# Kernel tuning notes

Measured on AMD Instinct MI355X. Metric: run time of the kernel, lower is better.

Reference implementation:

```python
import jax, jax.numpy as jnp
import numpy as np

B, T, D = 8, 512, 1024
S, H, TOPK = 2048, 4, 8
Dh = D // H
LR_FAST, LR_DEEP = 1.0, 0.1
SURPRISE_TH, DECAY = 0.6, 0.9995


def layer_norm(x, g, b, eps=1e-5):
    m = jnp.mean(x, -1, keepdims=True)
    v = jnp.var(x, -1, keepdims=True)
    return (x - m) * jax.lax.rsqrt(v + eps) * g + b


def setup_inputs() -> dict:
    key = jax.random.key(0)
    ks = jax.random.split(key, 8)
    s = 0.02
    f32 = jnp.float32
    return {
        "x": jax.random.normal(ks[0], (B, T, D), f32),
        "write_mask": jnp.ones((B, T), dtype=bool),
        # Mamba backbone stub: 2 residual MLP blocks (Linear d->2d, GELU, Linear 2d->d, LN)
        "W1": jax.random.normal(ks[1], (2, D, 2 * D), f32) * s,
        "b1": jnp.zeros((2, 2 * D), f32),
        "W2": jax.random.normal(ks[2], (2, 2 * D, D), f32) * s,
        "b2": jnp.zeros((2, D), f32),
        "ln_g": jnp.ones((2, D), f32),
        "ln_b": jnp.zeros((2, D), f32),
        # memory fusion
        "fuse_W": jax.random.normal(ks[3], (2 * D, D), f32) * s,
        "fuse_b": jnp.zeros((D,), f32),
        "mln_g": jnp.ones((D,), f32),
        "mln_b": jnp.zeros((D,), f32),
        # persistent DualTierMiras memory bank (keys / values)
        "mem_K": jax.random.normal(ks[4], (S, D), f32) * s,
        "mem_V": jax.random.normal(ks[5], (S, D), f32) * s,
    }


def _forward(x, write_mask, W1, b1, W2, b2, ln_g, ln_b, fuse_W, fuse_b, mln_g, mln_b, mem_K, mem_V):
    # --- Mamba backbone (vectorized over B,T) ---
    h = x
    for i in range(2):
        y = jax.nn.gelu(h @ W1[i] + b1[i]) @ W2[i] + b2[i]
        h = h + layer_norm(y, ln_g[i], ln_b[i])

    inv_sqrt_dh = 1.0 / np.sqrt(Dh).astype(np.float32)
    inv_sqrt_d = 1.0 / np.sqrt(D).astype(np.float32)

    def step(carry, inputs):
        mK, mV = carry                      # [S,D] each
        h_t, m_t = inputs                   # [B,D], [B] bool
        # --- top-k sparse multi-head memory read ---
        q = h_t.reshape(B, H, Dh)
        Kh = mK.reshape(S, H, Dh).transpose(1, 0, 2)   # [H,S,Dh]
        Vh = mV.reshape(S, H, Dh).transpose(1, 0, 2)   # [H,S,Dh]
        scores = jnp.einsum('bhd,hsd->bhs', q, Kh) * inv_sqrt_dh  # [B,H,S]
        topv, topi = jax.lax.top_k(scores, TOPK)                   # [B,H,K]
        w = jax.nn.softmax(topv, axis=-1)
        vals = jax.vmap(lambda v, i: v[i])(Vh, topi.transpose(1, 0, 2))  # [H,B,K,Dh]
        v_t = jnp.einsum('bhk,hbkd->bhd', w, vals).reshape(B, D)
        # --- residual fusion ---
        fused = jnp.concatenate([h_t, v_t], -1) @ fuse_W + fuse_b
        fused = layer_norm(fused + h_t, mln_g, mln_b)
        # --- surprise-gated EMA scatter write (detached, decayed) ---
        key_w = jax.lax.stop_gradient(h_t)
        val_w = jax.lax.stop_gradient(fused)
        sw = key_w @ mK.T * inv_sqrt_d                 # [B,S]
        p = jax.nn.softmax(sw, -1)
        slot = jnp.argmax(sw, -1)                      # [B]
        surprise = 1.0 - jnp.max(p, -1)                # [B]
        lr = jnp.where(surprise > SURPRISE_TH, LR_FAST, LR_DEEP)
        lr = lr * m_t.astype(lr.dtype)                 # per-sample write gate
        decay = jnp.where(jnp.any(m_t), DECAY, 1.0)
        mV2 = mV * decay
        mV2 = mV2.at[slot].add(lr[:, None] * (val_w - mV2[slot]))
        mK2 = mK.at[slot].add(lr[:, None] * (key_w - mK[slot]))
        return (mK2, mV2), fused

    (_, _), out = jax.lax.scan(step, (mem_K, mem_V), (h.transpose(1, 0, 2), write_mask.T))
    return out.transpose(1, 0, 2)   # [B,T,D]


def reference(x, write_mask, W1, b1, W2, b2, ln_g, ln_b, fuse_W, fuse_b, mln_g, mln_b, mem_K, mem_V):
    return _forward(x, write_mask, W1, b1, W2, b2, ln_g, ln_b, fuse_W, fuse_b, mln_g, mln_b, mem_K, mem_V)
```

## Files before the change

### kernel.cpp

```cpp
#include <hip/hip_runtime.h>
#include <cstdint>

#define TT 512
#define DD 1024
#define SS 2048
#define BB 8
#define DECAYF 0.9995f
#define NBLK 80

__device__ __forceinline__ float cldf(const float* p) {
  return __hip_atomic_load(p, __ATOMIC_RELAXED, __HIP_MEMORY_SCOPE_AGENT);
}
__device__ __forceinline__ void cstf(float* p, float v) {
  __hip_atomic_store(p, v, __ATOMIC_RELAXED, __HIP_MEMORY_SCOPE_AGENT);
}
__device__ __forceinline__ int cldi(const int* p) {
  return __hip_atomic_load(p, __ATOMIC_RELAXED, __HIP_MEMORY_SCOPE_AGENT);
}
__device__ __forceinline__ void csti(int* p, int v) {
  __hip_atomic_store(p, v, __ATOMIC_RELAXED, __HIP_MEMORY_SCOPE_AGENT);
}

template<int MODE, bool BT>
__global__ __launch_bounds__(256) void gemm64(
    const float* __restrict__ A, int lda,
    const float* __restrict__ B, int ldb,
    const float* __restrict__ bias,
    float* __restrict__ C, int ldc,
    const float* __restrict__ res, int resld,
    int K)
{
  __shared__ float As[16][68];
  __shared__ float Bs[16][68];
  const int tid = threadIdx.x;
  const int m0 = blockIdx.y * 64, n0 = blockIdx.x * 64;
  const int tx = tid & 15, ty = tid >> 4;
  const int a_r = tid >> 2, a_k = (tid & 3) * 4;
  const int b_k = tid >> 4, b_n = (tid & 15) * 4;
  float acc[4][4];
#pragma unroll
  for (int i = 0; i < 4; ++i)
#pragma unroll
    for (int j = 0; j < 4; ++j) acc[i][j] = 0.f;

  for (int k0 = 0; k0 < K; k0 += 16) {
    float4 av = *(const float4*)(A + (size_t)(m0 + a_r) * lda + k0 + a_k);
    As[a_k + 0][a_r] = av.x; As[a_k + 1][a_r] = av.y;
    As[a_k + 2][a_r] = av.z; As[a_k + 3][a_r] = av.w;
    if (!BT) {
      float4 bv = *(const float4*)(B + (size_t)(k0 + b_k) * ldb + n0 + b_n);
      Bs[b_k][b_n + 0] = bv.x; Bs[b_k][b_n + 1] = bv.y;
      Bs[b_k][b_n + 2] = bv.z; Bs[b_k][b_n + 3] = bv.w;
    } else {
      float4 bv = *(const float4*)(B + (size_t)(n0 + a_r) * ldb + k0 + a_k);
      Bs[a_k + 0][a_r] = bv.x; Bs[a_k + 1][a_r] = bv.y;
      Bs[a_k + 2][a_r] = bv.z; Bs[a_k + 3][a_r] = bv.w;
    }
    __syncthreads();
#pragma unroll
    for (int kk = 0; kk < 16; ++kk) {
      float4 a4 = *(const float4*)&As[kk][ty * 4];
      float4 b4 = *(const float4*)&Bs[kk][tx * 4];
      float aa[4] = {a4.x, a4.y, a4.z, a4.w};
      float bb[4] = {b4.x, b4.y, b4.z, b4.w};
#pragma unroll
      for (int i = 0; i < 4; ++i)
#pragma unroll
        for (int j = 0; j < 4; ++j) acc[i][j] += aa[i] * bb[j];
    }
    __syncthreads();
  }
#pragma unroll
  for (int i = 0; i < 4; ++i) {
    const int row = m0 + ty * 4 + i;
    const int col = n0 + tx * 4;
    float v[4];
#pragma unroll
    for (int j = 0; j < 4; ++j) {
      float x = acc[i][j];
      if (MODE == 0 || MODE == 1 || MODE == 3) x += bias[col + j];
      if (MODE == 1) {
        float t3 = x * x * x;
        x = 0.5f * x * (1.f + tanhf(0.7978845608028654f * (x + 0.044715f * t3)));
      }
      if (MODE == 3) x += res[(size_t)row * resld + col + j];
      v[j] = x;
    }
    float4 o; o.x = v[0]; o.y = v[1]; o.z = v[2]; o.w = v[3];
    *(float4*)(C + (size_t)row * ldc + col) = o;
  }
}

__global__ __launch_bounds__(256) void ln_residual(
    const float* __restrict__ Y, float* __restrict__ Hio,
    const float* __restrict__ g, const float* __restrict__ b)
{
  const int row = blockIdx.x, tid = threadIdx.x;
  const int lane = tid & 63, wid = tid >> 6;
  __shared__ float red[8];
  __shared__ float s_m, s_r;
  float x[4]; float ls = 0.f, lq = 0.f;
#pragma unroll
  for (int r = 0; r < 4; ++r) {
    x[r] = Y[(size_t)row * DD + tid + 256 * r];
    ls += x[r]; lq += x[r] * x[r];
  }
#pragma unroll
  for (int off = 32; off; off >>= 1) { ls += __shfl_down(ls, off); lq += __shfl_down(lq, off); }
  if (lane == 0) { red[wid] = ls; red[4 + wid] = lq; }
  __syncthreads();
  if (tid == 0) {
    float S = red[0] + red[1] + red[2] + red[3];
    float Q = red[4] + red[5] + red[6] + red[7];
    float mean = S * (1.f / 1024.f);
    float var = Q * (1.f / 1024.f) - mean * mean;
    s_m = mean; s_r = rsqrtf(var + 1e-5f);
  }
  __syncthreads();
#pragma unroll
  for (int r = 0; r < 4; ++r) {
    int d = tid + 256 * r;
    Hio[(size_t)row * DD + d] += (x[r] - s_m) * s_r * g[d] + b[d];
  }
}

__global__ void init_state(float* fst) {
  if (threadIdx.x == 0 && blockIdx.x == 0) { fst[0] = 1.f; fst[2] = 1.f; }
}

__device__ __forceinline__ void gbar(int* arr, int* gen, int ep, int bid) {
  const int tid = threadIdx.x;
  __syncthreads();
  if (bid == 0) {
    if (tid > 0 && tid < NBLK) {
      while (cldi(&arr[tid * 32]) < ep) __builtin_amdgcn_s_sleep(1);
    }
    __syncthreads();
    if (tid == 0) csti(gen, ep);
  } else {
    if (tid == 0) {
      csti(&arr[bid * 32], ep);
      while (cldi(gen) < ep) __builtin_amdgcn_s_sleep(1);
    }
  }
  __syncthreads();
}

__device__ __forceinline__ void fuse_ln_out(
    int b, int tl,
    const float* __restrict__ HP, const float* part,
    float* __restrict__ H, float* pval,
    const float* __restrict__ mg, const float* __restrict__ mb,
    float* xr, float* s_red)
{
  const int tid = threadIdx.x;
  const int lane = tid & 63, wid = tid >> 6;
  const size_t row = (size_t)b * TT + tl;
  float ls = 0.f, lq = 0.f;
#pragma unroll
  for (int r = 0; r < 4; ++r) {
    int d = tid + 256 * r;
    float x = HP[row * DD + d]
            + cldf(&part[(0 * 8 + b) * DD + d]) + cldf(&part[(1 * 8 + b) * DD + d])
            + cldf(&part[(2 * 8 + b) * DD + d]) + cldf(&part[(3 * 8 + b) * DD + d]);
    xr[d] = x; ls += x; lq += x * x;
  }
#pragma unroll
  for (int off = 32; off; off >>= 1) { ls += __shfl_down(ls, off); lq += __shfl_down(lq, off); }
  if (lane == 0) { s_red[wid] = ls; s_red[4 + wid] = lq; }
  __syncthreads();
  if (tid == 0) {
    float S = s_red[0] + s_red[1] + s_red[2] + s_red[3];
    float Q = s_red[4] + s_red[5] + s_red[6] + s_red[7];
    float mean = S * (1.f / 1024.f);
    float var = Q * (1.f / 1024.f) - mean * mean;
    s_red[8] = mean; s_red[9] = rsqrtf(var + 1e-5f);
  }
  __syncthreads();
  const float mean = s_red[8], rstd = s_red[9];
#pragma unroll
  for (int r = 0; r < 4; ++r) {
    int d = tid + 256 * r;
    float val = (xr[d] - mean) * rstd * mg[d] + mb[d];
    H[row * DD + d] = val;
    cstf(&pval[b * DD + d], val);
  }
}

__global__ __launch_bounds__(256) void scan_kernel(
    float* __restrict__ H, const float* __restrict__ R0, const float* __restrict__ HP,
    float* dK, float* U,
    float* fst, int* ist, int* gen, int* arr, int* dflag, int* dlist,
    float* coefg, float* vt, float* part, float* pval,
    const float* __restrict__ K0, const float* __restrict__ fuseW,
    const float* __restrict__ mg, const float* __restrict__ mb)
{
  const int bid = blockIdx.x;
  const int tid = threadIdx.x;
  const int lane = tid & 63, wid = tid >> 6;
  __shared__ float smem[4352];
  __shared__ float s_tkv[8];
  __shared__ int   s_tki[8];
  __shared__ float s_red[12];
  __shared__ int   s_redi[8];
  __shared__ float s_f0;
  __shared__ int   s_i0;

  for (int t = 0; t < TT; ++t) {
    const int p = t & 1, pp = p ^ 1;
    if (bid < 32) {
      const int b = bid >> 2, h = bid & 3;
      float* sc = smem;
      float* qh = smem + 2048;
      const size_t row = (size_t)b * TT + t;
      qh[tid] = H[row * DD + h * 256 + tid];
#pragma unroll
      for (int j = 0; j < 8; ++j) sc[tid + 256 * j] = 0.f;
      __syncthreads();
      const int nd = cldi(&ist[16]);
      for (int i = wid; i < nd; i += 4) {
        const int s = cldi(&dlist[i]);
        const float* dkp = dK + (size_t)s * DD + h * 256;
        float pa = 0.f;
#pragma unroll
        for (int r = 0; r < 4; ++r) { int d = lane + 64 * r; pa += qh[d] * cldf(&dkp[d]); }
#pragma unroll
        for (int off = 32; off; off >>= 1) pa += __shfl_down(pa, off);
        if (lane == 0) sc[s] = pa;
      }
      __syncthreads();
      const float* r0 = R0 + (row * 4 + h) * SS;
#pragma unroll
      for (int j = 0; j < 8; ++j) { int s = tid + 256 * j; sc[s] += r0[s]; }
      __syncthreads();
      if (wid == 0) {
        float a[32];
#pragma unroll
        for (int i = 0; i < 32; ++i) a[i] = sc[lane + 64 * i];
        unsigned msk = 0u;
        for (int r = 0; r < 8; ++r) {
          float bv = -3e38f; int bj = 0;
#pragma unroll
          for (int i = 0; i < 32; ++i) {
            bool ok = !((msk >> i) & 1u) && (a[i] > bv);
            bv = ok ? a[i] : bv;
            bj = ok ? i : bj;
          }
          int bidx = lane + 64 * bj;
#pragma unroll
          for (int off = 1; off < 64; off <<= 1) {
            float ov = __shfl_xor(bv, off);
            int oi = __shfl_xor(bidx, off);
            if (ov > bv || (ov == bv && oi < bidx)) { bv = ov; bidx = oi; }
          }
          if (lane == (bidx & 63)) msk |= 1u << (bidx >> 6);
          if (lane == 0) { s_tkv[r] = bv; s_tki[r] = bidx; }
        }
      }
      __syncthreads();
      float w8[8];
      {
        float mx = s_tkv[0], nrm = 0.f;
#pragma unroll
        for (int j = 0; j < 8; ++j) { w8[j] = __expf((s_tkv[j] - mx) * 0.0625f); nrm += w8[j]; }
        float scale = cldf(&fst[p]) / nrm;
#pragma unroll
        for (int j = 0; j < 8; ++j) w8[j] *= scale;
      }
      int psl[8]; float plr[8];
#pragma unroll
      for (int e = 0; e < 8; ++e) { psl[e] = cldi(&ist[pp * 8 + e]); plr[e] = cldf(&fst[4 + pp * 8 + e]); }
      float accv = 0.f;
#pragma unroll
      for (int j = 0; j < 8; ++j) {
        int idx = s_tki[j];
        float uval = cldf(&U[(size_t)idx * DD + h * 256 + tid]);
        float L = 0.f;
#pragma unroll
        for (int e = 0; e < 8; ++e) L += (psl[e] == idx) ? plr[e] : 0.f;
        accv += w8[j] * uval * (1.f - L);
      }
      cstf(&vt[b * DD + h * 256 + tid], accv);
      if (tid < 8) {
        int myslot = cldi(&ist[pp * 8 + tid]);
        float mylr = cldf(&fst[4 + pp * 8 + tid]);
        float ce = 0.f;
#pragma unroll
        for (int j = 0; j < 8; ++j) ce += (s_tki[j] == myslot) ? w8[j] : 0.f;
        cstf(&coefg[b * 32 + h * 8 + tid], ce * mylr * cldf(&fst[2 + p]));
      }
    } else if (bid < 40) {
      const int b = bid - 32;
      float* c2 = smem;
      float* qf = smem + 2048;
      const size_t row = (size_t)b * TT + t;
#pragma unroll
      for (int r = 0; r < 4; ++r) qf[tid + 256 * r] = H[row * DD + tid + 256 * r];
#pragma unroll
      for (int j = 0; j < 8; ++j) c2[tid + 256 * j] = 0.f;
      __syncthreads();
      const int nd = cldi(&ist[16]);
      for (int i = wid; i < nd; i += 4) {
        const int s = cldi(&dlist[i]);
        const float* dkp = dK + (size_t)s * DD;
        float pa = 0.f;
#pragma unroll
        for (int r = 0; r < 16; ++r) { int d = lane + 64 * r; pa += qf[d] * cldf(&dkp[d]); }
#pragma unroll
        for (int off = 32; off; off >>= 1) pa += __shfl_down(pa, off);
        if (lane == 0) c2[s] = pa;
      }
      __syncthreads();
      const float* r0 = R0 + row * 4 * SS;
      float sv[8];
#pragma unroll
      for (int j = 0; j < 8; ++j) {
        int s = tid + 256 * j;
        float raw = r0[s] + r0[SS + s] + r0[2 * SS + s] + r0[3 * SS + s] + c2[s];
        sv[j] = raw * 0.03125f;
      }
      float bv = -3e38f; int bi = 0;
#pragma unroll
      for (int j = 0; j < 8; ++j) {
        bool ok = sv[j] > bv;
        bi = ok ? tid + 256 * j : bi;
        bv = ok ? sv[j] : bv;
      }
#pragma unroll
      for (int off = 32; off; off >>= 1) {
        float ov = __shfl_down(bv, off);
        int oi = __shfl_down(bi, off);
        if (ov > bv || (ov == bv && oi < bi)) { bv = ov; bi = oi; }
      }
      if (lane == 0) { s_red[wid] = bv; s_redi[wid] = bi; }
      __syncthreads();
      if (tid == 0) {
#pragma unroll
        for (int w2 = 1; w2 < 4; ++w2)
          if (s_red[w2] > bv || (s_red[w2] == bv && s_redi[w2] < bi)) { bv = s_red[w2]; bi = s_redi[w2]; }
        s_f0 = bv; s_i0 = bi;
      }
      __syncthreads();
      const float m = s_f0;
      float es = 0.f;
#pragma unroll
      for (int j = 0; j < 8; ++j) es += __expf(sv[j] - m);
#pragma unroll
      for (int off = 32; off; off >>= 1) es += __shfl_down(es, off);
      if (lane == 0) s_red[4 + wid] = es;
      __syncthreads();
      if (tid == 0) {
        float se = s_red[4] + s_red[5] + s_red[6] + s_red[7];
        float surprise = 1.f - 1.f / se;
        cstf(&fst[4 + p * 8 + b], surprise > 0.6f ? 1.0f : 0.1f);
        csti(&ist[p * 8 + b], s_i0);
      }
    } else if (bid < 48) {
      if (t > 0) fuse_ln_out(bid - 40, t - 1, HP, part, H, pval, mg, mb, smem, s_red);
    }
    gbar(arr, gen, 2 * t + 1, bid);
    if (bid < 64) {
      const int g = bid >> 2, kc = bid & 3;
      float* vtl = smem;
      float* pr = smem + 2048;
      float* cfs = smem + 4096;
      cfs[tid] = cldf(&coefg[tid]);
      float pv[8];
#pragma unroll
      for (int e = 0; e < 8; ++e) pv[e] = cldf(&pval[e * DD + kc * 256 + tid]);
      __syncthreads();
#pragma unroll
      for (int r = 0; r < 8; ++r) {
        float v = cldf(&vt[r * DD + kc * 256 + tid]);
#pragma unroll
        for (int e = 0; e < 8; ++e) v += cfs[r * 32 + kc * 8 + e] * pv[e];
        vtl[r * 256 + tid] = v;
      }
      __syncthreads();
      const int colq = tid & 63, ksub = tid >> 6;
      const int col = 64 * g + colq;
      float acc[8];
#pragma unroll
      for (int b2 = 0; b2 < 8; ++b2) acc[b2] = 0.f;
      const float* W2 = fuseW + (size_t)(DD + kc * 256 + ksub * 64) * DD + col;
      const float* vl = vtl + ksub * 64;
      for (int kk = 0; kk < 64; ++kk) {
        float wv = W2[(size_t)kk * DD];
#pragma unroll
        for (int b2 = 0; b2 < 8; ++b2) acc[b2] += vl[b2 * 256 + kk] * wv;
      }
#pragma unroll
      for (int b2 = 0; b2 < 8; ++b2) pr[ksub * 512 + colq * 8 + b2] = acc[b2];
      __syncthreads();
      if (ksub == 0) {
#pragma unroll
        for (int b2 = 0; b2 < 8; ++b2) {
          float s2 = pr[colq * 8 + b2] + pr[512 + colq * 8 + b2]
                   + pr[1024 + colq * 8 + b2] + pr[1536 + colq * 8 + b2];
          cstf(&part[(kc * 8 + b2) * DD + col], s2);
        }
      }
    } else if (bid < 72) {
      const int e = bid - 64;
      int sl[8]; float lr8[8];
#pragma unroll
      for (int e2 = 0; e2 < 8; ++e2) { sl[e2] = cldi(&ist[p * 8 + e2]); lr8[e2] = cldf(&fst[4 + p * 8 + e2]); }
      const int s = sl[e];
      bool owner = true;
      for (int e2 = 0; e2 < e; ++e2) if (sl[e2] == s) owner = false;
      if (owner) {
        float L = 0.f;
#pragma unroll
        for (int e2 = 0; e2 < 8; ++e2) if (sl[e2] == s) L += lr8[e2];
#pragma unroll
        for (int r = 0; r < 4; ++r) {
          int d = tid + 256 * r;
          float add = 0.f;
#pragma unroll
          for (int e2 = 0; e2 < 8; ++e2)
            if (sl[e2] == s) add += lr8[e2] * H[((size_t)e2 * TT + t) * DD + d];
          size_t o = (size_t)s * DD + d;
          cstf(&dK[o], cldf(&dK[o]) * (1.f - L) - L * K0[o] + add);
        }
        if (tid == 0) {
          if (atomicCAS(&dflag[s], 0, 1) == 0) {
            int pidx = atomicAdd(&ist[16], 1);
            csti(&dlist[pidx], s);
          }
        }
      }
      if (bid == 64 && tid == 0) {
        float cn = cldf(&fst[p]) * DECAYF;
        cstf(&fst[pp], cn); cstf(&fst[2 + pp], 1.f / cn);
      }
    } else {
      const int e = bid - 72;
      int sl[8]; float lr8[8];
#pragma unroll
      for (int e2 = 0; e2 < 8; ++e2) { sl[e2] = cldi(&ist[pp * 8 + e2]); lr8[e2] = cldf(&fst[4 + pp * 8 + e2]); }
      const int s = sl[e];
      bool owner = true;
      for (int e2 = 0; e2 < e; ++e2) if (sl[e2] == s) owner = false;
      if (owner) {
        float L = 0.f;
#pragma unroll
        for (int e2 = 0; e2 < 8; ++e2) if (sl[e2] == s) L += lr8[e2];
        if (L > 0.f) {
          const float psv = cldf(&fst[2 + p]);
#pragma unroll
          for (int r = 0; r < 4; ++r) {
            int d = tid + 256 * r;
            float add = 0.f;
#pragma unroll
            for (int e2 = 0; e2 < 8; ++e2)
              if (sl[e2] == s) add += lr8[e2] * cldf(&pval[e2 * DD + d]);
            size_t o = (size_t)s * DD + d;
            cstf(&U[o], cldf(&U[o]) * (1.f - L) + psv * add);
          }
        }
      }
    }
    gbar(arr, gen, 2 * t + 2, bid);
  }
  if (bid >= 40 && bid < 48)
    fuse_ln_out(bid - 40, TT - 1, HP, part, H, pval, mg, mb, smem, s_red);
}

extern "C" void kernel_launch(void* const* d_in, const int* in_sizes, int n_in,
                              void* d_out, int out_size, void* d_ws, size_t ws_size,
                              hipStream_t stream) {
  (void)in_sizes; (void)n_in; (void)out_size; (void)ws_size;
  const float* x     = (const float*)d_in[0];
  const float* W1    = (const float*)d_in[2];
  const float* b1    = (const float*)d_in[3];
  const float* W2    = (const float*)d_in[4];
  const float* b2    = (const float*)d_in[5];
  const float* lng   = (const float*)d_in[6];
  const float* lnb   = (const float*)d_in[7];
  const float* fuseW = (const float*)d_in[8];
  const float* fuseB = (const float*)d_in[9];
  const float* mlng  = (const float*)d_in[10];
  const float* mlnb  = (const float*)d_in[11];
  const float* memK  = (const float*)d_in[12];
  const float* memV  = (const float*)d_in[13];

  float* H = (float*)d_out;
  char* w = (char*)d_ws;
  float* R0 = (float*)w;
  float* Y1 = (float*)w;
  float* Y2 = (float*)(w + (size_t)32 * 1024 * 1024);
  float* HP = (float*)(w + (size_t)128 * 1024 * 1024);
  float* dK = (float*)(w + (size_t)144 * 1024 * 1024);
  float* U  = (float*)(w + (size_t)152 * 1024 * 1024);
  char*  st = w + (size_t)160 * 1024 * 1024;
  float* fst   = (float*)st;
  int*   ist   = (int*)(st + 128);
  int*   gen   = (int*)(st + 256);
  int*   arr   = (int*)(st + 512);
  int*   dflag = (int*)(st + 12288);
  int*   dlist = (int*)(st + 20480);
  float* coefg = (float*)(st + 28672);
  float* vt    = (float*)(st + 32768);
  float* part  = (float*)(st + 65536);
  float* pval  = (float*)(st + 196608);

  hipMemcpyAsync(H, x, (size_t)BB * TT * DD * sizeof(float),
                 hipMemcpyDeviceToDevice, stream);
  for (int l = 0; l < 2; ++l) {
    gemm64<1, false><<<dim3(32, 64), 256, 0, stream>>>(
        H, 1024, W1 + (size_t)l * 1024 * 2048, 2048, b1 + l * 2048,
        Y1, 2048, nullptr, 0, 1024);
    gemm64<0, false><<<dim3(16, 64), 256, 0, stream>>>(
        Y1, 2048, W2 + (size_t)l * 2048 * 1024, 1024, b2 + l * 1024,
        Y2, 1024, nullptr, 0, 2048);
    ln_residual<<<4096, 256, 0, stream>>>(Y2, H, lng + l * 1024, lnb + l * 1024);
  }
  hipMemsetAsync(dK, 0, (size_t)8 * 1024 * 1024, stream);
  hipMemsetAsync(st, 0, 262144, stream);
  hipMemcpyAsync(U, memV, (size_t)8 * 1024 * 1024, hipMemcpyDeviceToDevice, stream);
  init_state<<<1, 1, 0, stream>>>(fst);
  for (int h = 0; h < 4; ++h) {
    gemm64<2, true><<<dim3(32, 64), 256, 0, stream>>>(
        H + h * 256, 1024, memK + h * 256, 1024, nullptr,
        R0 + h * 2048, 8192, nullptr, 0, 256);
  }
  gemm64<3, false><<<dim3(16, 64), 256, 0, stream>>>(
      H, 1024, fuseW, 1024, fuseB, HP, 1024, H, 1024, 1024);
  scan_kernel<<<NBLK, 256, 0, stream>>>(H, R0, HP, dK, U, fst, ist, gen, arr,
                                        dflag, dlist, coefg, vt, part, pval,
                                        memK, fuseW, mlng, mlnb);
}
```

Before: 15.51 ms.

## Precompute next-step delta-key corrections in idle blocks and batch coherent vector loads

Blocks 48-79, which previously sat idle in the first phase, now compute the dot products of the next timestep's query against all dirtied delta-key rows. They write these into a double-buffered corr array. The read-side blocks then only patch the up to 8 slots changed in the previous step, instead of looping over the full dirty list on the critical path. Scalar atomic loads are also replaced with batched inline-asm dwordx4 loads using sc0/sc1 cache bypass and one waitcnt, which increases memory-level parallelism. The cost is extra workspace, a larger memset, and correctness that depends on the hand-written cache-coherence asm and the correction ordering.

Result: faster. 14.33 ms (-7.6%).

```diff
diff --git a/kernel.cpp b/kernel.cpp
--- a/kernel.cpp
+++ b/kernel.cpp
@@ -8,6 +8,9 @@
 #define DECAYF 0.9995f
 #define NBLK 80
 
+typedef float f4 __attribute__((ext_vector_type(4)));
+typedef int   i4x __attribute__((ext_vector_type(4)));
+
 __device__ __forceinline__ float cldf(const float* p) {
   return __hip_atomic_load(p, __ATOMIC_RELAXED, __HIP_MEMORY_SCOPE_AGENT);
 }
@@ -20,6 +23,27 @@
 __device__ __forceinline__ void csti(int* p, int v) {
   __hip_atomic_store(p, v, __ATOMIC_RELAXED, __HIP_MEMORY_SCOPE_AGENT);
 }
+
+__device__ __forceinline__ void ild4(f4& v, const float* p) {
+  asm volatile("global_load_dwordx4 %0, %1, off sc0 sc1" : "=v"(v) : "v"(p));
+}
+__device__ __forceinline__ void ild1(float& v, const float* p) {
+  asm volatile("global_load_dword %0, %1, off sc0 sc1" : "=v"(v) : "v"(p));
+}
+__device__ __forceinline__ void ildi1(int& v, const int* p) {
+  asm volatile("global_load_dword %0, %1, off sc0 sc1" : "=v"(v) : "v"(p));
+}
+__device__ __forceinline__ void ildi4(i4x& v, const int* p) {
+  asm volatile("global_load_dwordx4 %0, %1, off sc0 sc1" : "=v"(v) : "v"(p));
+}
+__device__ __forceinline__ void st4c(float* p, f4 v) {
+  asm volatile("global_store_dwordx4 %0, %1, off sc0 sc1" :: "v"(p), "v"(v) : "memory");
+}
+__device__ __forceinline__ void vmwait() {
+  asm volatile("s_waitcnt vmcnt(0)" ::: "memory");
+}
+template <typename T>
+__device__ __forceinline__ void pin(T& v) { asm volatile("" : "+v"(v)); }
 
 template<int MODE, bool BT>
 __global__ __launch_bounds__(256) void gemm64(
@@ -130,6 +154,7 @@
 
 __device__ __forceinline__ void gbar(int* arr, int* gen, int ep, int bid) {
   const int tid = threadIdx.x;
+  vmwait();
   __syncthreads();
   if (bid == 0) {
     if (tid > 0 && tid < NBLK) {
@@ -151,20 +176,22 @@
     const float* __restrict__ HP, const float* part,
     float* __restrict__ H, float* pval,
     const float* __restrict__ mg, const float* __restrict__ mb,
-    float* xr, float* s_red)
+    float* s_red)
 {
   const int tid = threadIdx.x;
   const int lane = tid & 63, wid = tid >> 6;
   const size_t row = (size_t)b * TT + tl;
-  float ls = 0.f, lq = 0.f;
-#pragma unroll
-  for (int r = 0; r < 4; ++r) {
-    int d = tid + 256 * r;
-    float x = HP[row * DD + d]
-            + cldf(&part[(0 * 8 + b) * DD + d]) + cldf(&part[(1 * 8 + b) * DD + d])
-            + cldf(&part[(2 * 8 + b) * DD + d]) + cldf(&part[(3 * 8 + b) * DD + d]);
-    xr[d] = x; ls += x; lq += x * x;
-  }
+  const int d4 = 4 * tid;
+  f4 p0, p1, p2, p3;
+  ild4(p0, part + (size_t)(0 * 8 + b) * DD + d4);
+  ild4(p1, part + (size_t)(1 * 8 + b) * DD + d4);
+  ild4(p2, part + (size_t)(2 * 8 + b) * DD + d4);
+  ild4(p3, part + (size_t)(3 * 8 + b) * DD + d4);
+  f4 hp = *(const f4*)(HP + row * DD + d4);
+  vmwait(); pin(p0); pin(p1); pin(p2); pin(p3);
+  f4 x = hp + p0 + p1 + p2 + p3;
+  float ls = x.x + x.y + x.z + x.w;
+  float lq = x.x * x.x + x.y * x.y + x.z * x.z + x.w * x.w;
 #pragma unroll
   for (int off = 32; off; off >>= 1) { ls += __shfl_down(ls, off); lq += __shfl_down(lq, off); }
   if (lane == 0) { s_red[wid] = ls; s_red[4 + wid] = lq; }
@@ -178,60 +205,80 @@
   }
   __syncthreads();
   const float mean = s_red[8], rstd = s_red[9];
-#pragma unroll
-  for (int r = 0; r < 4; ++r) {
-    int d = tid + 256 * r;
-    float val = (xr[d] - mean) * rstd * mg[d] + mb[d];
-    H[row * DD + d] = val;
-    cstf(&pval[b * DD + d], val);
-  }
+  f4 g4 = *(const f4*)(mg + d4);
+  f4 b4 = *(const f4*)(mb + d4);
+  f4 val = (x - mean) * rstd * g4 + b4;
+  *(f4*)(H + row * DD + d4) = val;
+  st4c(pval + (size_t)b * DD + d4, val);
 }
 
 __global__ __launch_bounds__(256) void scan_kernel(
     float* __restrict__ H, const float* __restrict__ R0, const float* __restrict__ HP,
     float* dK, float* U,
     float* fst, int* ist, int* gen, int* arr, int* dflag, int* dlist,
-    float* coefg, float* vt, float* part, float* pval,
+    float* coefg, float* vt, float* part, float* pval, float* corr,
     const float* __restrict__ K0, const float* __restrict__ fuseW,
     const float* __restrict__ mg, const float* __restrict__ mb)
 {
   const int bid = blockIdx.x;
   const int tid = threadIdx.x;
   const int lane = tid & 63, wid = tid >> 6;
-  __shared__ float smem[4352];
+  __shared__ __align__(16) float smem[4352];
   __shared__ float s_tkv[8];
   __shared__ int   s_tki[8];
   __shared__ float s_red[12];
   __shared__ int   s_redi[8];
   __shared__ float s_f0;
   __shared__ int   s_i0;
+  const f4 fz = {0.f, 0.f, 0.f, 0.f};
 
   for (int t = 0; t < TT; ++t) {
     const int p = t & 1, pp = p ^ 1;
     if (bid < 32) {
       const int b = bid >> 2, h = bid & 3;
       float* sc = smem;
-      float* qh = smem + 2048;
       const size_t row = (size_t)b * TT + t;
-      qh[tid] = H[row * DD + h * 256 + tid];
-#pragma unroll
-      for (int j = 0; j < 8; ++j) sc[tid + 256 * j] = 0.f;
-      __syncthreads();
-      const int nd = cldi(&ist[16]);
-      for (int i = wid; i < nd; i += 4) {
-        const int s = cldi(&dlist[i]);
-        const float* dkp = dK + (size_t)s * DD + h * 256;
-        float pa = 0.f;
-#pragma unroll
-        for (int r = 0; r < 4; ++r) { int d = lane + 64 * r; pa += qh[d] * cldf(&dkp[d]); }
-#pragma unroll
-        for (int off = 32; off; off >>= 1) pa += __shfl_down(pa, off);
-        if (lane == 0) sc[s] = pa;
-      }
-      __syncthreads();
       const float* r0 = R0 + (row * 4 + h) * SS;
-#pragma unroll
-      for (int j = 0; j < 8; ++j) { int s = tid + 256 * j; sc[s] += r0[s]; }
+      const float* ch = corr + ((size_t)(p * 32 + b * 4 + h) << 11);
+      f4 c0, c1;
+      ild4(c0, ch + 4 * tid);
+      ild4(c1, ch + 4 * tid + 1024);
+      int psl[8]; float plr[8];
+#pragma unroll
+      for (int e = 0; e < 8; ++e) {
+        ildi1(psl[e], ist + pp * 8 + e);
+        ild1(plr[e], fst + 4 + pp * 8 + e);
+      }
+      float fscale, fpsv; int sf0, sf1;
+      ild1(fscale, fst + p);
+      ild1(fpsv, fst + 2 + p);
+      ildi1(sf0, ist + pp * 8 + wid * 2);
+      ildi1(sf1, ist + pp * 8 + wid * 2 + 1);
+      f4 ra = *(const f4*)(r0 + 4 * tid);
+      f4 rb = *(const f4*)(r0 + 4 * tid + 1024);
+      vmwait();
+      pin(c0); pin(c1);
+#pragma unroll
+      for (int e = 0; e < 8; ++e) { pin(psl[e]); pin(plr[e]); }
+      pin(fscale); pin(fpsv); pin(sf0); pin(sf1);
+      *(f4*)(sc + 4 * tid) = ra + c0;
+      *(f4*)(sc + 4 * tid + 1024) = rb + c1;
+      __syncthreads();
+      {
+        f4 qv = *(const f4*)(H + row * DD + h * 256 + 4 * lane);
+        f4 d0, d1;
+        ild4(d0, dK + (size_t)sf0 * DD + h * 256 + 4 * lane);
+        ild4(d1, dK + (size_t)sf1 * DD + h * 256 + 4 * lane);
+        vmwait(); pin(d0); pin(d1);
+        float pa = d0.x * qv.x + d0.y * qv.y + d0.z * qv.z + d0.w * qv.w;
+        float pb = d1.x * qv.x + d1.y * qv.y + d1.z * qv.z + d1.w * qv.w;
+#pragma unroll
+        for (int off = 32; off; off >>= 1) {
+          pa += __shfl_down(pa, off);
+          pb += __shfl_down(pb, off);
+        }
+        if (lane == 0) { sc[sf0] = r0[sf0] + pa; sc[sf1] = r0[sf1] + pb; }
+      }
       __syncthreads();
       if (wid == 0) {
         float a[32];
@@ -263,22 +310,25 @@
         float mx = s_tkv[0], nrm = 0.f;
 #pragma unroll
         for (int j = 0; j < 8; ++j) { w8[j] = __expf((s_tkv[j] - mx) * 0.0625f); nrm += w8[j]; }
-        float scale = cldf(&fst[p]) / nrm;
+        float scale = fscale / nrm;
 #pragma unroll
         for (int j = 0; j < 8; ++j) w8[j] *= scale;
       }
-      int psl[8]; float plr[8];
-#pragma unroll
-      for (int e = 0; e < 8; ++e) { psl[e] = cldi(&ist[pp * 8 + e]); plr[e] = cldf(&fst[4 + pp * 8 + e]); }
       float accv = 0.f;
+      int idx8[8]; float uv[8];
+#pragma unroll
+      for (int j = 0; j < 8; ++j) idx8[j] = s_tki[j];
+#pragma unroll
+      for (int j = 0; j < 8; ++j) ild1(uv[j], U + (size_t)idx8[j] * DD + h * 256 + tid);
+      vmwait();
+#pragma unroll
+      for (int j = 0; j < 8; ++j) pin(uv[j]);
 #pragma unroll
       for (int j = 0; j < 8; ++j) {
-        int idx = s_tki[j];
-        float uval = cldf(&U[(size_t)idx * DD + h * 256 + tid]);
         float L = 0.f;
 #pragma unroll
-        for (int e = 0; e < 8; ++e) L += (psl[e] == idx) ? plr[e] : 0.f;
-        accv += w8[j] * uval * (1.f - L);
+        for (int e = 0; e < 8; ++e) L += (psl[e] == idx8[j]) ? plr[e] : 0.f;
+        accv += w8[j] * uv[j] * (1.f - L);
       }
       cstf(&vt[b * DD + h * 256 + tid], accv);
       if (tid < 8) {
@@ -287,38 +337,74 @@
         float ce = 0.f;
 #pragma unroll
         for (int j = 0; j < 8; ++j) ce += (s_tki[j] == myslot) ? w8[j] : 0.f;
-        cstf(&coefg[b * 32 + h * 8 + tid], ce * mylr * cldf(&fst[2 + p]));
+        cstf(&coefg[b * 32 + h * 8 + tid], ce * mylr * fpsv);
       }
     } else if (bid < 40) {
       const int b = bid - 32;
-      float* c2 = smem;
-      float* qf = smem + 2048;
+      float* svl = smem;
       const size_t row = (size_t)b * TT + t;
-#pragma unroll
-      for (int r = 0; r < 4; ++r) qf[tid + 256 * r] = H[row * DD + tid + 256 * r];
-#pragma unroll
-      for (int j = 0; j < 8; ++j) c2[tid + 256 * j] = 0.f;
-      __syncthreads();
-      const int nd = cldi(&ist[16]);
-      for (int i = wid; i < nd; i += 4) {
-        const int s = cldi(&dlist[i]);
-        const float* dkp = dK + (size_t)s * DD;
-        float pa = 0.f;
-#pragma unroll
-        for (int r = 0; r < 16; ++r) { int d = lane + 64 * r; pa += qf[d] * cldf(&dkp[d]); }
-#pragma unroll
-        for (int off = 32; off; off >>= 1) pa += __shfl_down(pa, off);
-        if (lane == 0) c2[s] = pa;
-      }
-      __syncthreads();
       const float* r0 = R0 + row * 4 * SS;
+      f4 cc[8];
+#pragma unroll
+      for (int h2 = 0; h2 < 4; ++h2) {
+        const float* chh = corr + ((size_t)(p * 32 + b * 4 + h2) << 11);
+        ild4(cc[h2 * 2], chh + 4 * tid);
+        ild4(cc[h2 * 2 + 1], chh + 4 * tid + 1024);
+      }
+      int sf0, sf1;
+      ildi1(sf0, ist + pp * 8 + wid * 2);
+      ildi1(sf1, ist + pp * 8 + wid * 2 + 1);
+      f4 a0 = fz, a1 = fz;
+#pragma unroll
+      for (int h2 = 0; h2 < 4; ++h2) {
+        a0 += *(const f4*)(r0 + (size_t)h2 * SS + 4 * tid);
+        a1 += *(const f4*)(r0 + (size_t)h2 * SS + 4 * tid + 1024);
+      }
+      vmwait();
+#pragma unroll
+      for (int u = 0; u < 8; ++u) pin(cc[u]);
+      pin(sf0); pin(sf1);
+      a0 += cc[0] + cc[2] + cc[4] + cc[6];
+      a1 += cc[1] + cc[3] + cc[5] + cc[7];
+      *(f4*)(svl + 4 * tid) = a0;
+      *(f4*)(svl + 4 * tid + 1024) = a1;
+      __syncthreads();
+      {
+        const float* qrow = H + row * DD;
+        f4 q0 = *(const f4*)(qrow + 16 * lane);
+        f4 q1 = *(const f4*)(qrow + 16 * lane + 4);
+        f4 q2 = *(const f4*)(qrow + 16 * lane + 8);
+        f4 q3 = *(const f4*)(qrow + 16 * lane + 12);
+        const float* dp0 = dK + (size_t)sf0 * DD + 16 * lane;
+        const float* dp1 = dK + (size_t)sf1 * DD + 16 * lane;
+        f4 d0, d1, d2, d3, e0, e1, e2, e3;
+        ild4(d0, dp0); ild4(d1, dp0 + 4); ild4(d2, dp0 + 8); ild4(d3, dp0 + 12);
+        ild4(e0, dp1); ild4(e1, dp1 + 4); ild4(e2, dp1 + 8); ild4(e3, dp1 + 12);
+        vmwait();
+        pin(d0); pin(d1); pin(d2); pin(d3);
+        pin(e0); pin(e1); pin(e2); pin(e3);
+        float pa = d0.x*q0.x + d0.y*q0.y + d0.z*q0.z + d0.w*q0.w
+                 + d1.x*q1.x + d1.y*q1.y + d1.z*q1.z + d1.w*q1.w
+                 + d2.x*q2.x + d2.y*q2.y + d2.z*q2.z + d2.w*q2.w
+                 + d3.x*q3.x + d3.y*q3.y + d3.z*q3.z + d3.w*q3.w;
+        float pb = e0.x*q0.x + e0.y*q0.y + e0.z*q0.z + e0.w*q0.w
+                 + e1.x*q1.x + e1.y*q1.y + e1.z*q1.z + e1.w*q1.w
+                 + e2.x*q2.x + e2.y*q2.y + e2.z*q2.z + e2.w*q2.w
+                 + e3.x*q3.x + e3.y*q3.y + e3.z*q3.z + e3.w*q3.w;
+#pragma unroll
+        for (int off = 32; off; off >>= 1) {
+          pa += __shfl_down(pa, off);
+          pb += __shfl_down(pb, off);
+        }
+        if (lane == 0) {
+          svl[sf0] = r0[sf0] + r0[SS + sf0] + r0[2 * SS + sf0] + r0[3 * SS + sf0] + pa;
+          svl[sf1] = r0[sf1] + r0[SS + sf1] + r0[2 * SS + sf1] + r0[3 * SS + sf1] + pb;
+        }
+      }
+      __syncthreads();
       float sv[8];
 #pragma unroll
-      for (int j = 0; j < 8; ++j) {
-        int s = tid + 256 * j;
-        float raw = r0[s] + r0[SS + s] + r0[2 * SS + s] + r0[3 * SS + s] + c2[s];
-        sv[j] = raw * 0.03125f;
-      }
+      for (int j = 0; j < 8; ++j) sv[j] = svl[tid + 256 * j] * 0.03125f;
       float bv = -3e38f; int bi = 0;
 #pragma unroll
       for (int j = 0; j < 8; ++j) {
@@ -356,7 +442,45 @@
         csti(&ist[p * 8 + b], s_i0);
       }
     } else if (bid < 48) {
-      if (t > 0) fuse_ln_out(bid - 40, t - 1, HP, part, H, pval, mg, mb, smem, s_red);
+      if (t > 0) fuse_ln_out(bid - 40, t - 1, HP, part, H, pval, mg, mb, s_red);
+    } else {
+      if (t < TT - 1) {
+        const int j = bid - 48, b = j >> 2, h = j & 3;
+        int* sdl = (int*)smem;
+        i4x da, db;
+        ildi4(da, dlist + 8 * tid);
+        ildi4(db, dlist + 8 * tid + 4);
+        const int nd = cldi(&ist[16]);
+        f4 qv = *(const f4*)(H + ((size_t)b * TT + t + 1) * DD + h * 256 + 4 * lane);
+        vmwait(); pin(da); pin(db);
+        *(i4x*)(sdl + 8 * tid) = da;
+        *(i4x*)(sdl + 8 * tid + 4) = db;
+        __syncthreads();
+        float* cw = corr + ((size_t)(pp * 32 + b * 4 + h) << 11);
+        for (int m0 = wid; m0 < nd; m0 += 64) {
+          f4 buf[16]; int ss[16];
+#pragma unroll
+          for (int u = 0; u < 16; ++u) {
+            const int m = m0 + 4 * u;
+            const int s = sdl[m < nd ? m : m0];
+            ss[u] = (m < nd) ? s : -1;
+            ild4(buf[u], dK + (size_t)s * DD + h * 256 + 4 * lane);
+          }
+          vmwait();
+#pragma unroll
+          for (int u = 0; u < 16; ++u) pin(buf[u]);
+#pragma unroll
+          for (int u = 0; u < 16; ++u) {
+            if (ss[u] >= 0) {
+              float pa = buf[u].x * qv.x + buf[u].y * qv.y
+                       + buf[u].z * qv.z + buf[u].w * qv.w;
+#pragma unroll
+              for (int off = 32; off; off >>= 1) pa += __shfl_down(pa, off);
+              if (lane == 0) cstf(cw + ss[u], pa);
+            }
+          }
+        }
+      }
     }
     gbar(arr, gen, 2 * t + 1, bid);
     if (bid < 64) {
@@ -364,16 +488,23 @@
       float* vtl = smem;
       float* pr = smem + 2048;
       float* cfs = smem + 4096;
-      cfs[tid] = cldf(&coefg[tid]);
-      float pv[8];
-#pragma unroll
-      for (int e = 0; e < 8; ++e) pv[e] = cldf(&pval[e * DD + kc * 256 + tid]);
+      float pvv[8], vtv[8], cf1;
+#pragma unroll
+      for (int e = 0; e < 8; ++e) ild1(pvv[e], pval + (size_t)e * DD + kc * 256 + tid);
+#pragma unroll
+      for (int r = 0; r < 8; ++r) ild1(vtv[r], vt + (size_t)r * DD + kc * 256 + tid);
+      ild1(cf1, coefg + tid);
+      vmwait();
+#pragma unroll
+      for (int e = 0; e < 8; ++e) { pin(pvv[e]); pin(vtv[e]); }
+      pin(cf1);
+      cfs[tid] = cf1;
       __syncthreads();
 #pragma unroll
       for (int r = 0; r < 8; ++r) {
-        float v = cldf(&vt[r * DD + kc * 256 + tid]);
-#pragma unroll
-        for (int e = 0; e < 8; ++e) v += cfs[r * 32 + kc * 8 + e] * pv[e];
+        float v = vtv[r];
+#pragma unroll
+        for (int e = 0; e < 8; ++e) v += cfs[r * 32 + kc * 8 + e] * pvv[e];
         vtl[r * 256 + tid] = v;
       }
       __syncthreads();
@@ -402,26 +533,38 @@
       }
     } else if (bid < 72) {
       const int e = bid - 64;
-      int sl[8]; float lr8[8];
-#pragma unroll
-      for (int e2 = 0; e2 < 8; ++e2) { sl[e2] = cldi(&ist[p * 8 + e2]); lr8[e2] = cldf(&fst[4 + p * 8 + e2]); }
-      const int s = sl[e];
+      int sl[8]; float lr8[8]; int s;
+#pragma unroll
+      for (int e2 = 0; e2 < 8; ++e2) {
+        ildi1(sl[e2], ist + p * 8 + e2);
+        ild1(lr8[e2], fst + 4 + p * 8 + e2);
+      }
+      ildi1(s, ist + p * 8 + e);
+      vmwait();
+#pragma unroll
+      for (int e2 = 0; e2 < 8; ++e2) { pin(sl[e2]); pin(lr8[e2]); }
+      pin(s);
       bool owner = true;
-      for (int e2 = 0; e2 < e; ++e2) if (sl[e2] == s) owner = false;
+#pragma unroll
+      for (int e2 = 0; e2 < 8; ++e2) if (e2 < e && sl[e2] == s) owner = false;
       if (owner) {
         float L = 0.f;
 #pragma unroll
         for (int e2 = 0; e2 < 8; ++e2) if (sl[e2] == s) L += lr8[e2];
-#pragma unroll
-        for (int r = 0; r < 4; ++r) {
-          int d = tid + 256 * r;
-          float add = 0.f;
-#pragma unroll
-          for (int e2 = 0; e2 < 8; ++e2)
-            if (sl[e2] == s) add += lr8[e2] * H[((size_t)e2 * TT + t) * DD + d];
-          size_t o = (size_t)s * DD + d;
-          cstf(&dK[o], cldf(&dK[o]) * (1.f - L) - L * K0[o] + add);
-        }
+        const int d4 = 4 * tid;
+        f4 dk;
+        ild4(dk, dK + (size_t)s * DD + d4);
+        f4 k0 = *(const f4*)(K0 + (size_t)s * DD + d4);
+        f4 addv = fz;
+#pragma unroll
+        for (int e2 = 0; e2 < 8; ++e2)
+          if (sl[e2] == s) {
+            f4 hv = *(const f4*)(H + ((size_t)e2 * TT + t) * DD + d4);
+            addv += lr8[e2] * hv;
+          }
+        vmwait(); pin(dk);
+        f4 outv = dk * (1.f - L) - L * k0 + addv;
+        st4c(dK + (size_t)s * DD + d4, outv);
         if (tid == 0) {
           if (atomicCAS(&dflag[s], 0, 1) == 0) {
             int pidx = atomicAdd(&ist[16], 1);
@@ -435,35 +578,50 @@
       }
     } else {
       const int e = bid - 72;
-      int sl[8]; float lr8[8];
-#pragma unroll
-      for (int e2 = 0; e2 < 8; ++e2) { sl[e2] = cldi(&ist[pp * 8 + e2]); lr8[e2] = cldf(&fst[4 + pp * 8 + e2]); }
-      const int s = sl[e];
+      int sl[8]; float lr8[8]; int s; float psv;
+#pragma unroll
+      for (int e2 = 0; e2 < 8; ++e2) {
+        ildi1(sl[e2], ist + pp * 8 + e2);
+        ild1(lr8[e2], fst + 4 + pp * 8 + e2);
+      }
+      ildi1(s, ist + pp * 8 + e);
+      ild1(psv, fst + 2 + p);
+      vmwait();
+#pragma unroll
+      for (int e2 = 0; e2 < 8; ++e2) { pin(sl[e2]); pin(lr8[e2]); }
+      pin(s); pin(psv);
       bool owner = true;
-      for (int e2 = 0; e2 < e; ++e2) if (sl[e2] == s) owner = false;
+#pragma unroll
+      for (int e2 = 0; e2 < 8; ++e2) if (e2 < e && sl[e2] == s) owner = false;
       if (owner) {
         float L = 0.f;
 #pragma unroll
         for (int e2 = 0; e2 < 8; ++e2) if (sl[e2] == s) L += lr8[e2];
         if (L > 0.f) {
-          const float psv = cldf(&fst[2 + p]);
-#pragma unroll
-          for (int r = 0; r < 4; ++r) {
-            int d = tid + 256 * r;
-            float add = 0.f;
-#pragma unroll
-            for (int e2 = 0; e2 < 8; ++e2)
-              if (sl[e2] == s) add += lr8[e2] * cldf(&pval[e2 * DD + d]);
-            size_t o = (size_t)s * DD + d;
-            cstf(&U[o], cldf(&U[o]) * (1.f - L) + psv * add);
+          const int d4 = 4 * tid;
+          f4 uu, pb[8];
+          ild4(uu, U + (size_t)s * DD + d4);
+#pragma unroll
+          for (int e2 = 0; e2 < 8; ++e2) {
+            pb[e2] = fz;
+            if (sl[e2] == s) ild4(pb[e2], pval + (size_t)e2 * DD + d4);
           }
+          vmwait(); pin(uu);
+#pragma unroll
+          for (int e2 = 0; e2 < 8; ++e2) pin(pb[e2]);
+          f4 addv = fz;
+#pragma unroll
+          for (int e2 = 0; e2 < 8; ++e2)
+            if (sl[e2] == s) addv += lr8[e2] * pb[e2];
+          f4 outv = uu * (1.f - L) + psv * addv;
+          st4c(U + (size_t)s * DD + d4, outv);
         }
       }
     }
     gbar(arr, gen, 2 * t + 2, bid);
   }
   if (bid >= 40 && bid < 48)
-    fuse_ln_out(bid - 40, TT - 1, HP, part, H, pval, mg, mb, smem, s_red);
+    fuse_ln_out(bid - 40, TT - 1, HP, part, H, pval, mg, mb, s_red);
 }
 
 extern "C" void kernel_launch(void* const* d_in, const int* in_sizes, int n_in,
@@ -503,6 +661,7 @@
   float* vt    = (float*)(st + 32768);
   float* part  = (float*)(st + 65536);
   float* pval  = (float*)(st + 196608);
+  float* corr  = (float*)(st + 262144);
 
   hipMemcpyAsync(H, x, (size_t)BB * TT * DD * sizeof(float),
                  hipMemcpyDeviceToDevice, stream);
@@ -516,7 +675,7 @@
     ln_residual<<<4096, 256, 0, stream>>>(Y2, H, lng + l * 1024, lnb + l * 1024);
   }
   hipMemsetAsync(dK, 0, (size_t)8 * 1024 * 1024, stream);
-  hipMemsetAsync(st, 0, 262144, stream);
+  hipMemsetAsync(st, 0, 786432, stream);
   hipMemcpyAsync(U, memV, (size_t)8 * 1024 * 1024, hipMemcpyDeviceToDevice, stream);
   init_state<<<1, 1, 0, stream>>>(fst);
   for (int h = 0; h < 4; ++h) {
@@ -527,6 +686,6 @@
   gemm64<3, false><<<dim3(16, 64), 256, 0, stream>>>(
       H, 1024, fuseW, 1024, fuseB, HP, 1024, H, 1024, 1024);
   scan_kernel<<<NBLK, 256, 0, stream>>>(H, R0, HP, dK, U, fst, ist, gen, arr,
-                                        dflag, dlist, coefg, vt, part, pval,
+                                        dflag, dlist, coefg, vt, part, pval, corr,
                                         memK, fuseW, mlng, mlnb);
 }
```
